# Performance work log

Hardware: AMD Instinct MI355X
Metric: run time of the kernel (lower is better)

Reference implementation:

```python
import jax, jax.numpy as jnp
import numpy as np

DIM = 1536
NH = 12
HD = DIM // NH          # 128
C = HD // 2             # 64 rotary pairs
F, H, W = 6, 20, 20
L = F * H * W           # 2400
B = 1
MAX_POS = 1024
EPS = 1e-6


def _rope_freqs():
    """[MAX_POS, C, 2, 2] rotation matrices, split [22,21,21] across f/h/w axes."""
    c0 = C - 2 * (C // 3)           # 22
    c1 = C // 3                      # 21
    pos = np.arange(MAX_POS, dtype=np.float32)
    parts = []
    for m in (c0, c1, c1):
        inv = 1.0 / (10000.0 ** (np.arange(m, dtype=np.float32) / m))
        parts.append(pos[:, None] * inv[None, :])
    ang = np.concatenate(parts, axis=1)          # [MAX_POS, C]
    cos, sin = np.cos(ang), np.sin(ang)
    # R[..., j, k]: rows [cos, -sin], [sin, cos]
    R = np.stack([np.stack([cos, -sin], -1), np.stack([sin, cos], -1)], -2)
    return jnp.asarray(R, dtype=jnp.float32)


def setup_inputs() -> dict:
    key = jax.random.key(0)
    ks = jax.random.split(key, 12)
    s = 1.0 / np.sqrt(DIM)
    lin = lambda k: (jax.random.normal(k, (DIM, DIM), jnp.float32) * s)
    return {
        "x": jax.random.normal(ks[0], (B, L, DIM), jnp.float32),
        "Wq": lin(ks[1]), "bq": jax.random.normal(ks[2], (DIM,), jnp.float32) * 0.01,
        "Wk": lin(ks[3]), "bk": jax.random.normal(ks[4], (DIM,), jnp.float32) * 0.01,
        "Wv": lin(ks[5]), "bv": jax.random.normal(ks[6], (DIM,), jnp.float32) * 0.01,
        "Wo": lin(ks[7]), "bo": jax.random.normal(ks[8], (DIM,), jnp.float32) * 0.01,
        "gq": jnp.ones((DIM,), jnp.float32),
        "gk": jnp.ones((DIM,), jnp.float32),
        "seq_lens": jnp.full((B,), L, dtype=jnp.int32),
        "grid_sizes": jnp.asarray([[F, H, W]], dtype=jnp.int32),
        "freqs": _rope_freqs(),
    }


def _rms_norm(x, g, eps=EPS):
    # WanRMSNorm: x * rsqrt(mean(x^2, -1) + eps) * weight
    return x * jax.lax.rsqrt(jnp.mean(jnp.square(x), axis=-1, keepdims=True) + eps) * g


def _rope_apply(xh, grid_sizes, freqs):
    """xh: [B, L, n, d]; freqs: [MAX_POS, c, 2, 2]. All samples share one grid."""
    b, l, n, d = xh.shape
    c = d // 2
    c0 = c - 2 * (c // 3)
    c1 = c // 3
    f, h, w = (int(v) for v in np.asarray(grid_sizes[0]))
    # build per-position 3D rotation matrices: [f*h*w, c, 2, 2]
    fa = jnp.broadcast_to(freqs[:f, :c0][:, None, None], (f, h, w, c0, 2, 2))
    fb = jnp.broadcast_to(freqs[:h, c0:c0 + c1][None, :, None], (f, h, w, c1, 2, 2))
    fc = jnp.broadcast_to(freqs[:w, c0 + c1:c][None, None, :], (f, h, w, c1, 2, 2))
    R = jnp.concatenate([fa, fb, fc], axis=3).reshape(f * h * w, c, 2, 2)
    xp = xh.reshape(b, l, n, c, 2)
    out = jnp.einsum('lcjk,blnck->blncj', R, xp)
    return out.reshape(b, l, n, d)


def reference(x, Wq, bq, Wk, bk, Wv, bv, Wo, bo, gq, gk, seq_lens, grid_sizes, freqs):
    b, l = x.shape[:2]
    q = _rms_norm(x @ Wq.T + bq, gq).reshape(b, l, NH, HD)
    k = _rms_norm(x @ Wk.T + bk, gk).reshape(b, l, NH, HD)
    v = (x @ Wv.T + bv).reshape(b, l, NH, HD)
    q = _rope_apply(q, grid_sizes, freqs)
    k = _rope_apply(k, grid_sizes, freqs)
    # full attention with key-length mask (window_size=(-1,-1))
    scores = jnp.einsum('bqnd,bknd->bnqk', q, k) / np.sqrt(HD)
    kmask = jnp.arange(l)[None, :] < seq_lens[:, None]          # [B, L]
    scores = jnp.where(kmask[:, None, None, :], scores, -1e9)
    attn = jax.nn.softmax(scores, axis=-1)
    out = jnp.einsum('bnqk,bknd->bqnd', attn, v).reshape(b, l, DIM)
    return out @ Wo.T + bo
```

## Files before the change

kernel.cpp:

```cpp
#include <hip/hip_runtime.h>
#include <hip/hip_bf16.h>
#include <stdint.h>


#define DIM  1536
#define NH   12
#define HD   128
#define LSEQ 2400
#define LPAD 2432
#define KT2  32
#define NT2  (LPAD / KT2)
#define NTQ  19

typedef __attribute__((ext_vector_type(8))) short short8;
typedef __attribute__((ext_vector_type(8))) _Float16 half8;
typedef __attribute__((ext_vector_type(4))) float f32x4;
typedef unsigned short ushort_t;
typedef unsigned int   uint32;

__device__ __forceinline__ ushort_t f2bf(float f) {
  union { float f; unsigned u; } v; v.f = f;
  unsigned r = (v.u + 0x7fffu + ((v.u >> 16) & 1u)) >> 16;
  return (ushort_t)r;
}
__device__ __forceinline__ float bf2f(ushort_t h) {
  union { unsigned u; float f; } v; v.u = ((unsigned)h) << 16;
  return v.f;
}
__device__ __forceinline__ void async16(void* lds, const void* g) {
  __builtin_amdgcn_global_load_lds(
      (const __attribute__((address_space(1))) uint32*)g,
      (__attribute__((address_space(3))) uint32*)lds, 16, 0, 0);
}
__device__ __forceinline__ uint4 pack8(const float* f) {
  uint4 u;
  u.x = (uint32)f2bf(f[0]) | ((uint32)f2bf(f[1]) << 16);
  u.y = (uint32)f2bf(f[2]) | ((uint32)f2bf(f[3]) << 16);
  u.z = (uint32)f2bf(f[4]) | ((uint32)f2bf(f[5]) << 16);
  u.w = (uint32)f2bf(f[6]) | ((uint32)f2bf(f[7]) << 16);
  return u;
}

__global__ void cvt_all(const float* __restrict__ x,
                        const float* __restrict__ W0, const float* __restrict__ W1,
                        const float* __restrict__ W2, const float* __restrict__ W3,
                        ushort_t* __restrict__ xd,
                        ushort_t* __restrict__ d0, ushort_t* __restrict__ d1,
                        ushort_t* __restrict__ d2, ushort_t* __restrict__ d3)
{
  const int z = blockIdx.y;
  const int i = blockIdx.x * 256 + threadIdx.x;
  if (z == 0) {
    uint4 u = {0, 0, 0, 0};
    if (i * 8 < LSEQ * DIM) {
      float f[8];
      *(float4*)f = *(const float4*)(x + i * 8);
      *(float4*)(f + 4) = *(const float4*)(x + i * 8 + 4);
      u = pack8(f);
    }
    *(uint4*)(xd + i * 8) = u;
    return;
  }
  if (blockIdx.x >= DIM * DIM / 2048) return;
  const float* s = (z == 1) ? W0 : ((z == 2) ? W1 : ((z == 3) ? W2 : W3));
  ushort_t* d    = (z == 1) ? d0 : ((z == 2) ? d1 : ((z == 3) ? d2 : d3));
  float f[8];
  *(float4*)f = *(const float4*)(s + i * 8);
  *(float4*)(f + 4) = *(const float4*)(s + i * 8 + 4);
  *(uint4*)(d + i * 8) = pack8(f);
}

template<int OUT_F32>
__global__ __launch_bounds__(256) void gemm_bt(
    const ushort_t* __restrict__ Ap,
    const ushort_t* __restrict__ B0, const ushort_t* __restrict__ B1, const ushort_t* __restrict__ B2,
    const float* __restrict__ b0, const float* __restrict__ b1, const float* __restrict__ b2,
    void* __restrict__ D0, void* __restrict__ D1, void* __restrict__ D2,
    int Mout)
{
  const int z = blockIdx.y;
  const ushort_t* Bw  = (z == 0) ? B0 : ((z == 1) ? B1 : B2);
  const float* bias   = (z == 0) ? b0 : ((z == 1) ? b1 : b2);
  void* D             = (z == 0) ? D0 : ((z == 1) ? D1 : D2);

  const int bm = blockIdx.x / 12, bn = blockIdx.x % 12;
  const int tid = threadIdx.x;
  const int w = tid >> 6, lam = tid & 63;
  const int wr = w >> 1, wc = w & 1;
  const int lane15 = lam & 15, quad = lam >> 4;

  __shared__ __align__(16) char lds[32768];
  char* sA = lds;
  char* sB = lds + 16384;

  f32x4 acc[4][4];
#pragma unroll
  for (int i = 0; i < 4; ++i)
#pragma unroll
    for (int j = 0; j < 4; ++j) acc[i][j] = {};

  const int sm = (w * 32) + (lam >> 3);
  const int sc = (lam & 7);

  for (int k0 = 0; k0 < DIM; k0 += 64) {
    __syncthreads();
#pragma unroll
    for (int i = 0; i < 4; ++i) {
      const int li = w * 4096 + i * 1024;
      const int m = sm + i * 8;
      const int c = sc ^ (m & 7);
      async16(sA + li, Ap + (size_t)(bm * 128 + m) * DIM + k0 + c * 8);
      async16(sB + li, Bw + (size_t)(bn * 128 + m) * DIM + k0 + c * 8);
    }
    __syncthreads();
#pragma unroll
    for (int kc = 0; kc < 2; ++kc) {
      const int chunk = kc * 4 + quad;
      short8 af[4], bfr[4];
#pragma unroll
      for (int i = 0; i < 4; ++i) {
        const int m = wr * 64 + i * 16 + lane15;
        af[i] = *(const short8*)(sA + m * 128 + ((chunk ^ (m & 7)) * 16));
      }
#pragma unroll
      for (int j = 0; j < 4; ++j) {
        const int n = wc * 64 + j * 16 + lane15;
        bfr[j] = *(const short8*)(sB + n * 128 + ((chunk ^ (n & 7)) * 16));
      }
#pragma unroll
      for (int i = 0; i < 4; ++i)
#pragma unroll
        for (int j = 0; j < 4; ++j)
          acc[i][j] = __builtin_amdgcn_mfma_f32_16x16x32_bf16(af[i], bfr[j], acc[i][j], 0, 0, 0);
    }
  }

#pragma unroll
  for (int j = 0; j < 4; ++j) {
    const int n = bn * 128 + wc * 64 + j * 16 + lane15;
    const float bv = bias[n];
#pragma unroll
    for (int i = 0; i < 4; ++i) {
      const int mb = bm * 128 + wr * 64 + i * 16 + quad * 4;
#pragma unroll
      for (int r = 0; r < 4; ++r) {
        const int m = mb + r;
        const float val = acc[i][j][r] + bv;
        if (OUT_F32) {
          if (m < Mout) ((float*)D)[(size_t)m * DIM + n] = val;
        } else {
          ((ushort_t*)D)[(size_t)m * DIM + n] = f2bf(val);
        }
      }
    }
  }
}

__global__ __launch_bounds__(256) void nr_vp(
    const ushort_t* __restrict__ qpre, const ushort_t* __restrict__ kpre,
    const ushort_t* __restrict__ vbf,
    const float* __restrict__ gq, const float* __restrict__ gk,
    const float* __restrict__ freqs,
    const int* __restrict__ seq_lens, const int* __restrict__ grid_sizes,
    ushort_t* __restrict__ qh, ushort_t* __restrict__ kh,
    ushort_t* __restrict__ vp)
{
  const int bx = blockIdx.x;
  const int tid = threadIdx.x;
  __shared__ float wsum[4];
  __shared__ float srstd;
  __shared__ ushort_t tbuf[32][33];

  if (bx >= 2 * LPAD) {
    const int vb = bx - 2 * LPAD;
    const int head = vb / (NT2 * 4);
    const int rem = vb - head * (NT2 * 4);
    const int t2 = rem >> 2;
    const int d0 = (rem & 3) * 32;
    const int l0 = t2 * 32;
    const int tx = tid & 31, ty = tid >> 5;
#pragma unroll
    for (int rr = 0; rr < 4; ++rr)
      tbuf[ty * 4 + rr][tx] = vbf[(size_t)(l0 + ty * 4 + rr) * DIM + head * HD + d0 + tx];
    __syncthreads();
#pragma unroll
    for (int rr = 0; rr < 4; ++rr) {
      const int d = d0 + ty * 4 + rr;
      vp[(((size_t)head * NT2 + t2) * HD + d) * KT2 + tx] = tbuf[tx][ty * 4 + rr];
    }
    return;
  }

  const int row = bx >> 1;
  const int which = bx & 1;
  const ushort_t* src = which ? kpre : qpre;
  const float* g = which ? gk : gq;
  ushort_t* dst = which ? kh : qh;

  float s = 0.f;
  if (tid < 192) {
    uint4 u = *(const uint4*)(src + (size_t)row * DIM + tid * 8);
    const uint32 uu[4] = {u.x, u.y, u.z, u.w};
#pragma unroll
    for (int i = 0; i < 4; ++i) {
      float a = bf2f((ushort_t)(uu[i] & 0xffff));
      float b = bf2f((ushort_t)(uu[i] >> 16));
      s += a * a + b * b;
    }
  }
#pragma unroll
  for (int off = 32; off; off >>= 1) s += __shfl_down(s, off, 64);
  if ((tid & 63) == 0) wsum[tid >> 6] = s;
  __syncthreads();
  if (tid == 0)
    srstd = rsqrtf((wsum[0] + wsum[1] + wsum[2] + wsum[3]) / (float)DIM + 1e-6f);
  __syncthreads();
  const float rstd = srstd;

  const int seq = seq_lens[0];
  const int h_ = grid_sizes[1], w_ = grid_sizes[2];
  const int hw = h_ * w_;
  const int fidx = row / hw;
  const int rem = row - fidx * hw;
  const int hidx = rem / w_;
  const int widx = rem - hidx * w_;
  const bool live = row < seq;

#pragma unroll
  for (int pp = 0; pp < 3; ++pp) {
    const int p = tid + pp * 256;
    const int c = p & 63, head = p >> 6;
    const int e_in = head * HD + 2 * c;
    uint32 xin = *(const uint32*)(src + (size_t)row * DIM + e_in);
    float x0 = bf2f((ushort_t)(xin & 0xffff));
    float x1 = bf2f((ushort_t)(xin >> 16));
    float2 gg = *(const float2*)(g + e_in);
    float y0 = x0 * rstd * gg.x, y1 = x1 * rstd * gg.y;
    const int pos = (c < 22) ? fidx : ((c < 43) ? hidx : widx);
    float4 R = *(const float4*)(freqs + ((size_t)pos * 64 + c) * 4);
    float o0 = R.x * y0 + R.y * y1;
    float o1 = R.z * y0 + R.w * y1;
    uint32 op = live ? ((uint32)f2bf(o0) | ((uint32)f2bf(o1) << 16)) : 0u;
    *(uint32*)(dst + ((size_t)head * LPAD + row) * HD + 2 * c) = op;
  }
}

__global__ __launch_bounds__(256, 3) void attn7(
    const ushort_t* __restrict__ qh, const ushort_t* __restrict__ kh,
    const ushort_t* __restrict__ vp, const int* __restrict__ seq_lens,
    _Float16* __restrict__ op0, _Float16* __restrict__ op1,
    _Float16* __restrict__ op2, _Float16* __restrict__ op3,
    float* __restrict__ lp)
{
  const int qz = blockIdx.z;
  const int head = blockIdx.y;
  const int q0 = blockIdx.x * 128;
  const int tid = threadIdx.x;
  const int w = tid >> 6, lam = tid & 63;
  const int lane15 = lam & 15, quad = lam >> 4;
  const int seq = seq_lens[0];
  _Float16* op = (qz == 0) ? op0 : ((qz == 1) ? op1 : ((qz == 2) ? op2 : op3));

  __shared__ __align__(16) char kbuf[2][8192];
  __shared__ __align__(16) char vbuf[2][8192];
  __shared__ __align__(16) ushort_t pbuf[4][32][40];

  const ushort_t* qbase = qh + ((size_t)head * LPAD + q0 + w * 32) * HD;
  short8 qf[2][4];
#pragma unroll
  for (int qt = 0; qt < 2; ++qt)
#pragma unroll
    for (int kc = 0; kc < 4; ++kc)
      qf[qt][kc] = *(const short8*)(qbase + (qt * 16 + lane15) * HD + kc * 32 + quad * 8);

  f32x4 o[2][8];
#pragma unroll
  for (int qt = 0; qt < 2; ++qt)
#pragma unroll
    for (int dt = 0; dt < 8; ++dt) o[qt][dt] = {};
  float lacc[2][4] = {};

  const float scale = 0.08838834764831845f;

  const ushort_t* khh = kh + (size_t)head * LPAD * HD;
  const ushort_t* vph = vp + (size_t)head * NT2 * HD * KT2;

  const int krow0 = w * 8 + (lam >> 4);
  const int kslot = lam & 15;

#define STAGE(gt, b)                                                     \
  {                                                                      \
    const ushort_t* kg = khh + (size_t)(gt) * (KT2 * HD);                \
    const ushort_t* vg = vph + (size_t)(gt) * (HD * KT2);                \
    _Pragma("unroll")                                                    \
    for (int i = 0; i < 2; ++i) {                                        \
      const int li = w * 2048 + i * 1024;                                \
      const int kr = krow0 + i * 4;                                      \
      const int kc_ = kslot ^ (kr & 15);                                 \
      async16(kbuf[b] + li, kg + kr * HD + kc_ * 8);                     \
      const int G = w * 128 + i * 64 + lam;                              \
      const int l_ = (G >> 2) & 15;                                      \
      const int cc = (G & 3) ^ (l_ & 3);                                 \
      const int d_ = ((G >> 6) << 4) + l_;                               \
      async16(vbuf[b] + li, vg + d_ * KT2 + cc * 8);                     \
    }                                                                    \
  }

  const int tbase = qz * NTQ;
  STAGE(tbase, 0)
  __syncthreads();

  for (int t = 0; t < NTQ; ++t) {
    const int b = t & 1;
    const int gt = tbase + t;
    if (t + 1 < NTQ) STAGE(gt + 1, b ^ 1)

    f32x4 S[2][2];
    S[0][0] = {}; S[0][1] = {}; S[1][0] = {}; S[1][1] = {};
#pragma unroll
    for (int n0 = 0; n0 < 2; ++n0)
#pragma unroll
      for (int kc = 0; kc < 4; ++kc) {
        short8 kf = *(const short8*)(kbuf[b] + (n0 * 16 + lane15) * 256 +
                                     (((kc * 4 + quad) ^ lane15) * 16));
#pragma unroll
        for (int qt = 0; qt < 2; ++qt)
          S[qt][n0] = __builtin_amdgcn_mfma_f32_16x16x32_bf16(qf[qt][kc], kf, S[qt][n0], 0, 0, 0);
      }

#pragma unroll
    for (int n0 = 0; n0 < 2; ++n0) {
      const bool valid = (gt * KT2 + n0 * 16 + lane15) < seq;
#pragma unroll
      for (int qt = 0; qt < 2; ++qt)
#pragma unroll
        for (int r = 0; r < 4; ++r) {
          float e = valid ? __expf(S[qt][n0][r] * scale - 12.0f) : 0.f;
          lacc[qt][r] += e;
          pbuf[w][qt * 16 + quad * 4 + r][n0 * 16 + lane15] = f2bf(e);
        }
    }
    asm volatile("s_waitcnt lgkmcnt(0)" ::: "memory");

    short8 pf[2];
#pragma unroll
    for (int qt = 0; qt < 2; ++qt)
      pf[qt] = *(const short8*)(&pbuf[w][qt * 16 + lane15][quad * 8]);
#pragma unroll
    for (int dt = 0; dt < 8; ++dt) {
      short8 vf = *(const short8*)(vbuf[b] + dt * 1024 +
                                   (lane15 * 4 + (quad ^ (lane15 & 3))) * 16);
#pragma unroll
      for (int qt = 0; qt < 2; ++qt)
        o[qt][dt] = __builtin_amdgcn_mfma_f32_16x16x32_bf16(pf[qt], vf, o[qt][dt], 0, 0, 0);
    }
    __syncthreads();
  }
#undef STAGE

#pragma unroll
  for (int qt = 0; qt < 2; ++qt) {
    float lrow[4], linv[4];
#pragma unroll
    for (int r = 0; r < 4; ++r) {
      float l = lacc[qt][r];
#pragma unroll
      for (int off = 1; off < 16; off <<= 1) l += __shfl_xor(l, off, 16);
      lrow[r] = l;
      linv[r] = 1.0f / l;
    }
    if (lane15 == 0) {
#pragma unroll
      for (int r = 0; r < 4; ++r)
        lp[((size_t)qz * NH + head) * LPAD + q0 + w * 32 + qt * 16 + quad * 4 + r] = lrow[r];
    }
#pragma unroll
    for (int dt = 0; dt < 8; ++dt)
#pragma unroll
      for (int r = 0; r < 4; ++r) {
        const int m = q0 + w * 32 + qt * 16 + quad * 4 + r;
        op[(size_t)m * DIM + head * HD + dt * 16 + lane15] =
            (_Float16)(o[qt][dt][r] * linv[r]);
      }
  }
}

__global__ void merge(const _Float16* __restrict__ o0, const _Float16* __restrict__ o1,
                      const _Float16* __restrict__ o2, const _Float16* __restrict__ o3,
                      const float* __restrict__ lp, ushort_t* __restrict__ attno)
{
  const int i = blockIdx.x * 256 + threadIdx.x;
  const int e = i * 8;
  const int m = e / DIM;
  const int head = (e - m * DIM) >> 7;
  float l[4];
#pragma unroll
  for (int h = 0; h < 4; ++h) l[h] = lp[((size_t)h * NH + head) * LPAD + m];
  const float inv = 1.0f / (l[0] + l[1] + l[2] + l[3]);
  half8 a = *(const half8*)(o0 + e);
  half8 b = *(const half8*)(o1 + e);
  half8 c = *(const half8*)(o2 + e);
  half8 d = *(const half8*)(o3 + e);
  const float w0 = l[0] * inv, w1 = l[1] * inv, w2 = l[2] * inv, w3 = l[3] * inv;
  float f[8];
#pragma unroll
  for (int j = 0; j < 8; ++j)
    f[j] = (float)a[j] * w0 + (float)b[j] * w1 + (float)c[j] * w2 + (float)d[j] * w3;
  *(uint4*)(attno + e) = pack8(f);
}

extern "C" void kernel_launch(void* const* d_in, const int* in_sizes, int n_in,
                              void* d_out, int out_size, void* d_ws, size_t ws_size,
                              hipStream_t stream)
{
  const float* x  = (const float*)d_in[0];
  const float* Wq = (const float*)d_in[1];
  const float* bq = (const float*)d_in[2];
  const float* Wk = (const float*)d_in[3];
  const float* bk = (const float*)d_in[4];
  const float* Wv = (const float*)d_in[5];
  const float* bv = (const float*)d_in[6];
  const float* Wo = (const float*)d_in[7];
  const float* bo = (const float*)d_in[8];
  const float* gq = (const float*)d_in[9];
  const float* gk = (const float*)d_in[10];
  const int* seq_lens   = (const int*)d_in[11];
  const int* grid_sizes = (const int*)d_in[12];
  const float* freqs    = (const float*)d_in[13];
  float* out = (float*)d_out;

  const size_t BUF = (size_t)LPAD * DIM * 2;
  const size_t WB  = (size_t)DIM * DIM * 2;
  char* ws = (char*)d_ws;
  dim3 blk(256);

  ushort_t* xbf  = (ushort_t*)(ws);
  ushort_t* wqb  = (ushort_t*)(ws + BUF);
  ushort_t* wkb  = (ushort_t*)(ws + BUF + WB);
  ushort_t* wvb  = (ushort_t*)(ws + BUF + 2 * WB);
  ushort_t* wob  = (ushort_t*)(ws + BUF + 3 * WB);
  ushort_t* qpre = (ushort_t*)(ws + BUF + 4 * WB);
  ushort_t* kpre = (ushort_t*)(ws + 2 * BUF + 4 * WB);
  ushort_t* qh   = (ushort_t*)(ws + 3 * BUF + 4 * WB);
  ushort_t* kh   = (ushort_t*)(ws + 4 * BUF + 4 * WB);
  ushort_t* vbf  = (ushort_t*)(ws + 5 * BUF + 4 * WB);
  ushort_t* vp    = xbf;
  ushort_t* attno = xbf;
  _Float16* op0 = (_Float16*)qpre;
  _Float16* op1 = (_Float16*)kpre;
  _Float16* op2 = (_Float16*)vbf;
  _Float16* op3 = (_Float16*)wqb;
  float*    lp  = (float*)wvb;

  cvt_all<<<dim3(LPAD * DIM / 2048, 5), blk, 0, stream>>>(
      x, Wq, Wk, Wv, Wo, xbf, wqb, wkb, wvb, wob);
  gemm_bt<0><<<dim3(228, 3), blk, 0, stream>>>(
      xbf, wqb, wkb, wvb, bq, bk, bv, qpre, kpre, vbf, 0);
  nr_vp<<<dim3(2 * LPAD + NH * NT2 * 4), blk, 0, stream>>>(
      qpre, kpre, vbf, gq, gk, freqs, seq_lens, grid_sizes, qh, kh, vp);
  attn7<<<dim3(LPAD / 128, NH, 4), blk, 0, stream>>>(
      qh, kh, vp, seq_lens, op0, op1, op2, op3, lp);
  merge<<<dim3(LPAD * DIM / 2048), blk, 0, stream>>>(op0, op1, op2, op3, lp, attno);
  gemm_bt<1><<<dim3(228, 1), blk, 0, stream>>>(
      attno, wob, wob, wob, bo, bo, bo, out, out, out, LSEQ);
}
```

Baseline: 296.4 us.

## Keep attention probabilities in registers via transposed QK MFMA and fp16 PV

The QK^T MFMA now uses swapped operands, so each lane holds scores for one query row across four keys. The exponentiated probabilities can then feed the PV MFMA directly as fp16 operands, with no round trip through the LDS pbuf. V is stored as fp16 in a permuted key order to match, exp uses exp2 with a folded scale and offset, and masking only runs on the tail tile. The cost is twice as many smaller 16x16x16 f16 MFMAs for PV, plus fp16 round-toward-zero conversion of the probabilities.

```diff
diff --git a/kernel.cpp b/kernel.cpp
--- a/kernel.cpp
+++ b/kernel.cpp
@@ -13,7 +13,9 @@
 #define NTQ  19
 
 typedef __attribute__((ext_vector_type(8))) short short8;
-typedef __attribute__((ext_vector_type(8))) _Float16 half8;
+typedef __attribute__((ext_vector_type(8))) __fp16 half8;
+typedef __attribute__((ext_vector_type(4))) __fp16 half4;
+typedef __attribute__((ext_vector_type(2))) __fp16 half2v;
 typedef __attribute__((ext_vector_type(4))) float f32x4;
 typedef unsigned short ushort_t;
 typedef unsigned int   uint32;
@@ -183,10 +185,13 @@
     for (int rr = 0; rr < 4; ++rr)
       tbuf[ty * 4 + rr][tx] = vbf[(size_t)(l0 + ty * 4 + rr) * DIM + head * HD + d0 + tx];
     __syncthreads();
+    const int kk = ((tx & 15) >> 2) * 8 + (tx & 3) + ((tx >> 4) & 1) * 4;
 #pragma unroll
     for (int rr = 0; rr < 4; ++rr) {
       const int d = d0 + ty * 4 + rr;
-      vp[(((size_t)head * NT2 + t2) * HD + d) * KT2 + tx] = tbuf[tx][ty * 4 + rr];
+      union { __fp16 h; ushort_t u; } cv;
+      cv.h = (__fp16)bf2f(tbuf[tx][ty * 4 + rr]);
+      vp[(((size_t)head * NT2 + t2) * HD + d) * KT2 + kk] = cv.u;
     }
     return;
   }
@@ -245,7 +250,7 @@
   }
 }
 
-__global__ __launch_bounds__(256, 3) void attn7(
+__global__ __launch_bounds__(256, 3) void attn8(
     const ushort_t* __restrict__ qh, const ushort_t* __restrict__ kh,
     const ushort_t* __restrict__ vp, const int* __restrict__ seq_lens,
     _Float16* __restrict__ op0, _Float16* __restrict__ op1,
@@ -263,7 +268,6 @@
 
   __shared__ __align__(16) char kbuf[2][8192];
   __shared__ __align__(16) char vbuf[2][8192];
-  __shared__ __align__(16) ushort_t pbuf[4][32][40];
 
   const ushort_t* qbase = qh + ((size_t)head * LPAD + q0 + w * 32) * HD;
   short8 qf[2][4];
@@ -278,9 +282,10 @@
   for (int qt = 0; qt < 2; ++qt)
 #pragma unroll
     for (int dt = 0; dt < 8; ++dt) o[qt][dt] = {};
-  float lacc[2][4] = {};
-
-  const float scale = 0.08838834764831845f;
+  float lacc[2] = {0.f, 0.f};
+
+  const float C1 = 0.12752540f;
+  const float C2 = -5.7707802f;
 
   const ushort_t* khh = kh + (size_t)head * LPAD * HD;
   const ushort_t* vph = vp + (size_t)head * NT2 * HD * KT2;
@@ -325,34 +330,42 @@
                                      (((kc * 4 + quad) ^ lane15) * 16));
 #pragma unroll
         for (int qt = 0; qt < 2; ++qt)
-          S[qt][n0] = __builtin_amdgcn_mfma_f32_16x16x32_bf16(qf[qt][kc], kf, S[qt][n0], 0, 0, 0);
-      }
-
-#pragma unroll
-    for (int n0 = 0; n0 < 2; ++n0) {
-      const bool valid = (gt * KT2 + n0 * 16 + lane15) < seq;
-#pragma unroll
-      for (int qt = 0; qt < 2; ++qt)
-#pragma unroll
-        for (int r = 0; r < 4; ++r) {
-          float e = valid ? __expf(S[qt][n0][r] * scale - 12.0f) : 0.f;
-          lacc[qt][r] += e;
-          pbuf[w][qt * 16 + quad * 4 + r][n0 * 16 + lane15] = f2bf(e);
+          S[qt][n0] = __builtin_amdgcn_mfma_f32_16x16x32_bf16(kf, qf[qt][kc], S[qt][n0], 0, 0, 0);
+      }
+
+    const bool tail = (gt == NT2 - 1);
+    half4 pf[2][2];
+#pragma unroll
+    for (int qt = 0; qt < 2; ++qt)
+#pragma unroll
+      for (int n0 = 0; n0 < 2; ++n0) {
+        float e[4];
+#pragma unroll
+        for (int r = 0; r < 4; ++r)
+          e[r] = exp2f(fmaf(S[qt][n0][r], C1, C2));
+        if (tail) {
+#pragma unroll
+          for (int r = 0; r < 4; ++r)
+            if (gt * KT2 + n0 * 16 + quad * 4 + r >= seq) e[r] = 0.f;
         }
-    }
-    asm volatile("s_waitcnt lgkmcnt(0)" ::: "memory");
-
-    short8 pf[2];
-#pragma unroll
-    for (int qt = 0; qt < 2; ++qt)
-      pf[qt] = *(const short8*)(&pbuf[w][qt * 16 + lane15][quad * 8]);
+        lacc[qt] += (e[0] + e[1]) + (e[2] + e[3]);
+        half2v lo = __builtin_amdgcn_cvt_pkrtz(e[0], e[1]);
+        half2v hi = __builtin_amdgcn_cvt_pkrtz(e[2], e[3]);
+        half4 pp = {lo[0], lo[1], hi[0], hi[1]};
+        pf[qt][n0] = pp;
+      }
+
 #pragma unroll
     for (int dt = 0; dt < 8; ++dt) {
-      short8 vf = *(const short8*)(vbuf[b] + dt * 1024 +
-                                   (lane15 * 4 + (quad ^ (lane15 & 3))) * 16);
-#pragma unroll
-      for (int qt = 0; qt < 2; ++qt)
-        o[qt][dt] = __builtin_amdgcn_mfma_f32_16x16x32_bf16(pf[qt], vf, o[qt][dt], 0, 0, 0);
+      half8 vv = *(const half8*)(vbuf[b] + dt * 1024 +
+                                 (lane15 * 4 + (quad ^ (lane15 & 3))) * 16);
+      half4 vlo = {vv[0], vv[1], vv[2], vv[3]};
+      half4 vhi = {vv[4], vv[5], vv[6], vv[7]};
+#pragma unroll
+      for (int qt = 0; qt < 2; ++qt) {
+        o[qt][dt] = __builtin_amdgcn_mfma_f32_16x16x16f16(vlo, pf[qt][0], o[qt][dt], 0, 0, 0);
+        o[qt][dt] = __builtin_amdgcn_mfma_f32_16x16x16f16(vhi, pf[qt][1], o[qt][dt], 0, 0, 0);
+      }
     }
     __syncthreads();
   }
@@ -360,28 +373,22 @@
 
 #pragma unroll
   for (int qt = 0; qt < 2; ++qt) {
-    float lrow[4], linv[4];
-#pragma unroll
-    for (int r = 0; r < 4; ++r) {
-      float l = lacc[qt][r];
-#pragma unroll
-      for (int off = 1; off < 16; off <<= 1) l += __shfl_xor(l, off, 16);
-      lrow[r] = l;
-      linv[r] = 1.0f / l;
-    }
-    if (lane15 == 0) {
-#pragma unroll
-      for (int r = 0; r < 4; ++r)
-        lp[((size_t)qz * NH + head) * LPAD + q0 + w * 32 + qt * 16 + quad * 4 + r] = lrow[r];
-    }
-#pragma unroll
-    for (int dt = 0; dt < 8; ++dt)
-#pragma unroll
-      for (int r = 0; r < 4; ++r) {
-        const int m = q0 + w * 32 + qt * 16 + quad * 4 + r;
-        op[(size_t)m * DIM + head * HD + dt * 16 + lane15] =
-            (_Float16)(o[qt][dt][r] * linv[r]);
-      }
+    float l = lacc[qt];
+    l += __shfl_xor(l, 16, 64);
+    l += __shfl_xor(l, 32, 64);
+    const float linv = 1.0f / l;
+    const int qrow = q0 + w * 32 + qt * 16 + lane15;
+    if (quad == 0)
+      lp[((size_t)qz * NH + head) * LPAD + qrow] = l;
+#pragma unroll
+    for (int dt = 0; dt < 8; ++dt) {
+      half2v a = __builtin_amdgcn_cvt_pkrtz(o[qt][dt][0] * linv, o[qt][dt][1] * linv);
+      half2v c = __builtin_amdgcn_cvt_pkrtz(o[qt][dt][2] * linv, o[qt][dt][3] * linv);
+      uint2 st;
+      st.x = __builtin_bit_cast(uint32, a);
+      st.y = __builtin_bit_cast(uint32, c);
+      *(uint2*)(op + (size_t)qrow * DIM + head * HD + dt * 16 + quad * 4) = st;
+    }
   }
 }
 
@@ -458,7 +465,7 @@
       xbf, wqb, wkb, wvb, bq, bk, bv, qpre, kpre, vbf, 0);
   nr_vp<<<dim3(2 * LPAD + NH * NT2 * 4), blk, 0, stream>>>(
       qpre, kpre, vbf, gq, gk, freqs, seq_lens, grid_sizes, qh, kh, vp);
-  attn7<<<dim3(LPAD / 128, NH, 4), blk, 0, stream>>>(
+  attn8<<<dim3(LPAD / 128, NH, 4), blk, 0, stream>>>(
       qh, kh, vp, seq_lens, op0, op1, op2, op3, lp);
   merge<<<dim3(LPAD * DIM / 2048), blk, 0, stream>>>(op0, op1, op2, op3, lp, attno);
   gemm_bt<1><<<dim3(228, 1), blk, 0, stream>>>(
```

Result: slower. 304.0 us (+2.5%).
